# Kernel tuning notes

Hardware: AMD Instinct MI355X
Metric: run time of the kernel (lower is better)

The kernel has to match this reference:

```python
import jax, jax.numpy as jnp
import numpy as np

ALPHA = 0.2          # LeakyReLU negative slope
MASK_VAL = -9e15     # matches torch -9000000000000000.0


def setup_inputs() -> dict:
    key = jax.random.key(0)
    k1, k2, k3, k4 = jax.random.split(key, 4)
    B, N, F_IN, F_OUT, DEG = 64, 1024, 64, 64, 8
    atoms = jax.random.normal(k1, (B, N, F_IN), dtype=jnp.float32)
    edges = jax.random.randint(k2, (B, N, DEG), 0, N, dtype=jnp.int64)
    # xavier_uniform with gain=1.414
    def xavier(k, shape, gain=1.414):
        fan_in, fan_out = shape[0], shape[1]
        bound = gain * np.sqrt(6.0 / (fan_in + fan_out))
        return jax.random.uniform(k, shape, jnp.float32, -bound, bound)
    W = xavier(k3, (F_IN, F_OUT))
    a = xavier(k4, (2 * F_OUT, 1))
    return {"atoms": atoms, "edges": edges, "W": W, "a": a}


def reference(atoms, edges, W, a):
    B, N, _ = atoms.shape
    F_OUT = W.shape[1]
    # h = atom @ W per graph -> [B, N, F_OUT]
    h = jnp.einsum('bnf,fo->bno', atoms, W)
    # Decompose concat-attention: e_ij = leakyrelu(h_i . a1 + h_j . a2)
    a1 = a[:F_OUT, 0]
    a2 = a[F_OUT:, 0]
    s1 = h @ a1  # [B, N]
    s2 = h @ a2  # [B, N]
    e = s1[:, :, None] + s2[:, None, :]  # [B, N, N]
    e = jnp.where(e > 0, e, ALPHA * e)   # LeakyReLU
    # Build adjacency mask from edge lists: adj[b, i, edges[b,i,d]] = True
    b_idx = jnp.arange(B)[:, None, None]
    i_idx = jnp.arange(N)[None, :, None]
    adj = jnp.zeros((B, N, N), dtype=bool).at[b_idx, i_idx, edges].set(True)
    e = jnp.where(adj, e, MASK_VAL)
    attn = jax.nn.softmax(e, axis=-1)    # [B, N, N]
    h_prime = jnp.einsum('bij,bjo->bio', attn, h)
    return jax.nn.elu(h_prime)
```

## Files before the change

kernel.cpp:

```cpp
#include <hip/hip_runtime.h>
#include <math.h>

#define BATCH 64
#define NNODE 1024
#define FDIM 64
#define DEG 8
#define ALPHA 0.2f

typedef __attribute__((ext_vector_type(8))) short bf16x8;
typedef __attribute__((ext_vector_type(4))) float f32x4;

__device__ __forceinline__ short f2bf(float f) {
    union { float f; unsigned u; } v; v.f = f;
    unsigned r = v.u + 0x7fffu + ((v.u >> 16) & 1u);
    return (short)(r >> 16);
}

__global__ void gat_k0(const float* __restrict__ W, const float* __restrict__ a,
                       float* __restrict__ wa) {
    const int k = threadIdx.x;
    float p1 = 0.f, p2 = 0.f;
    #pragma unroll
    for (int j = 0; j < FDIM; ++j) {
        const float w = W[k * FDIM + j];
        p1 = fmaf(w, a[j], p1);
        p2 = fmaf(w, a[FDIM + j], p2);
    }
    wa[k] = p1; wa[FDIM + k] = p2;
}

__global__ __launch_bounds__(256) void gat_k1(
    const float* __restrict__ atoms,
    const float* __restrict__ W,
    const float* __restrict__ wa,
    float* __restrict__ h,
    float* __restrict__ s1,
    float* __restrict__ s2)
{
    const int lane = threadIdx.x & 63;
    const int wv   = threadIdx.x >> 6;
    const int l16  = lane & 15;
    const int qd   = lane >> 4;
    const int rowbase = (blockIdx.x * 4 + wv) * 16;

    bf16x8 Bw[2][4];
    #pragma unroll
    for (int ks = 0; ks < 2; ++ks)
        #pragma unroll
        for (int t = 0; t < 4; ++t)
            #pragma unroll
            for (int j = 0; j < 8; ++j)
                Bw[ks][t][j] = f2bf(W[(ks * 32 + qd * 8 + j) * FDIM + t * 16 + l16]);

    bf16x8 Bs[2];
    #pragma unroll
    for (int ks = 0; ks < 2; ++ks)
        #pragma unroll
        for (int j = 0; j < 8; ++j) {
            const int k = ks * 32 + qd * 8 + j;
            const float v = (l16 == 0) ? wa[k] : ((l16 == 1) ? wa[FDIM + k] : 0.f);
            Bs[ks][j] = f2bf(v);
        }

    const float* __restrict__ ar = atoms + (size_t)(rowbase + l16) * FDIM;
    bf16x8 A[2];
    #pragma unroll
    for (int ks = 0; ks < 2; ++ks) {
        const float4 p0 = *(const float4*)(ar + ks * 32 + qd * 8);
        const float4 p1 = *(const float4*)(ar + ks * 32 + qd * 8 + 4);
        A[ks][0] = f2bf(p0.x); A[ks][1] = f2bf(p0.y);
        A[ks][2] = f2bf(p0.z); A[ks][3] = f2bf(p0.w);
        A[ks][4] = f2bf(p1.x); A[ks][5] = f2bf(p1.y);
        A[ks][6] = f2bf(p1.z); A[ks][7] = f2bf(p1.w);
    }

    f32x4 C[4] = {{0,0,0,0},{0,0,0,0},{0,0,0,0},{0,0,0,0}};
    f32x4 Cs = {0,0,0,0};
    #pragma unroll
    for (int ks = 0; ks < 2; ++ks) {
        #pragma unroll
        for (int t = 0; t < 4; ++t)
            C[t] = __builtin_amdgcn_mfma_f32_16x16x32_bf16(A[ks], Bw[ks][t], C[t], 0, 0, 0);
        Cs = __builtin_amdgcn_mfma_f32_16x16x32_bf16(A[ks], Bs[ks], Cs, 0, 0, 0);
    }

    #pragma unroll
    for (int t = 0; t < 4; ++t)
        #pragma unroll
        for (int r = 0; r < 4; ++r)
            h[(size_t)(rowbase + qd * 4 + r) * FDIM + t * 16 + l16] = C[t][r];

    if (l16 < 2) {
        float* sp = (l16 == 0) ? s1 : s2;
        #pragma unroll
        for (int r = 0; r < 4; ++r)
            sp[rowbase + qd * 4 + r] = Cs[r];
    }
}

__global__ __launch_bounds__(256) void gat_k2(
    const float* __restrict__ h,
    const float* __restrict__ s1g,
    const float* __restrict__ s2g,
    const int*   __restrict__ edges,
    float* __restrict__ out)
{
    __shared__ float s2l[NNODE];
    __shared__ int   el[64 * DEG];
    __shared__ float s1l[64];

    const int bid   = blockIdx.x;
    const int slot  = bid >> 3;
    const int b     = (bid & 7) + 8 * (slot & 7);
    const int chunk = slot >> 3;
    const int rowbase = b * NNODE + chunk * 64;

    const int tid = threadIdx.x;
    ((float4*)s2l)[tid] = ((const float4*)(s2g + b * NNODE))[tid];
    ((int2*)el)[tid]    = ((const int2*)(edges + (size_t)rowbase * DEG))[tid];
    if (tid < 64) s1l[tid] = s1g[rowbase + tid];
    __syncthreads();

    const int lane = tid & 63;
    const int wv   = tid >> 6;
    const float* __restrict__ hb = h + (size_t)b * NNODE * FDIM;

    #pragma unroll 2
    for (int i = 0; i < 16; ++i) {
        const int rl = wv * 16 + i;
        int ej[DEG];
        #pragma unroll
        for (int k = 0; k < DEG; ++k) ej[k] = el[rl * DEG + k];

        const float si = s1l[rl];
        float e[DEG], mx = -INFINITY;
        #pragma unroll
        for (int k = 0; k < DEG; ++k) {
            float v = si + s2l[ej[k]];
            v = (v > 0.f) ? v : ALPHA * v;
            e[k] = v; mx = fmaxf(mx, v);
        }
        float wgt[DEG], wsum = 0.f;
        #pragma unroll
        for (int k = 0; k < DEG; ++k) {
            bool kp = true;
            #pragma unroll
            for (int m = 0; m < DEG; ++m)
                if (m < k && ej[m] == ej[k]) kp = false;
            const float w = kp ? __expf(e[k] - mx) : 0.f;
            wgt[k] = w; wsum += w;
        }
        const float inv = 1.f / wsum;

        float acc = 0.f;
        #pragma unroll
        for (int k = 0; k < DEG; ++k)
            acc = fmaf(wgt[k] * inv, hb[(size_t)ej[k] * FDIM + lane], acc);

        out[(size_t)(rowbase + rl) * FDIM + lane] = (acc > 0.f) ? acc : (__expf(acc) - 1.f);
    }
}

extern "C" void kernel_launch(void* const* d_in, const int* in_sizes, int n_in,
                              void* d_out, int out_size, void* d_ws, size_t ws_size,
                              hipStream_t stream) {
    const float* atoms = (const float*)d_in[0];
    const int*   edges = (const int*)d_in[1];
    const float* W     = (const float*)d_in[2];
    const float* a     = (const float*)d_in[3];
    float* out = (float*)d_out;

    const int rows = BATCH * NNODE;

    float* h  = (float*)d_ws;
    float* s1 = h + (size_t)rows * FDIM;
    float* s2 = s1 + rows;
    float* wa = s2 + rows;

    gat_k0<<<1, 64, 0, stream>>>(W, a, wa);
    gat_k1<<<rows / 64, 256, 0, stream>>>(atoms, W, wa, h, s1, s2);
    gat_k2<<<rows / 64, 256, 0, stream>>>(h, s1, s2, edges, out);
}
```

Before: 102.7 us.

## Fuse projection, score and attention kernels into one LDS-resident per-graph kernel

```diff
diff --git a/kernel.cpp b/kernel.cpp
--- a/kernel.cpp
+++ b/kernel.cpp
@@ -6,6 +6,8 @@
 #define FDIM 64
 #define DEG 8
 #define ALPHA 0.2f
+#define HSTR 66
+#define WSTR 65
 
 typedef __attribute__((ext_vector_type(8))) short bf16x8;
 typedef __attribute__((ext_vector_type(4))) float f32x4;
@@ -15,33 +17,51 @@
     unsigned r = v.u + 0x7fffu + ((v.u >> 16) & 1u);
     return (short)(r >> 16);
 }
-
-__global__ void gat_k0(const float* __restrict__ W, const float* __restrict__ a,
-                       float* __restrict__ wa) {
-    const int k = threadIdx.x;
-    float p1 = 0.f, p2 = 0.f;
-    #pragma unroll
-    for (int j = 0; j < FDIM; ++j) {
-        const float w = W[k * FDIM + j];
-        p1 = fmaf(w, a[j], p1);
-        p2 = fmaf(w, a[FDIM + j], p2);
-    }
-    wa[k] = p1; wa[FDIM + k] = p2;
+__device__ __forceinline__ float bf2f(unsigned short s) {
+    union { unsigned u; float f; } v; v.u = ((unsigned)s) << 16;
+    return v.f;
 }
 
-__global__ __launch_bounds__(256) void gat_k1(
+__global__ __launch_bounds__(1024) void gat_fused(
     const float* __restrict__ atoms,
+    const int*   __restrict__ edges,
     const float* __restrict__ W,
-    const float* __restrict__ wa,
-    float* __restrict__ h,
-    float* __restrict__ s1,
-    float* __restrict__ s2)
+    const float* __restrict__ a,
+    float* __restrict__ out)
 {
-    const int lane = threadIdx.x & 63;
-    const int wv   = threadIdx.x >> 6;
+    extern __shared__ char smem[];
+    unsigned short* hl  = (unsigned short*)smem;
+    float*          Wl  = (float*)(smem + NNODE * HSTR * 2);
+    float*          s1l = Wl + FDIM * WSTR;
+    float*          s2l = s1l + NNODE;
+    float*          waL = s2l + NNODE;
+
+    const int tid = threadIdx.x;
+    const int bid = blockIdx.x;
+    const int xcd = bid & 7, kk = bid >> 3;
+    const int b     = xcd * 8 + (kk & 7);
+    const int chunk = kk >> 3;
+
+    #pragma unroll
+    for (int i = 0; i < 4; ++i) {
+        const int idx = tid + 1024 * i;
+        Wl[(idx >> 6) * WSTR + (idx & 63)] = W[idx];
+    }
+    __syncthreads();
+
+    const int lane = tid & 63;
+    const int wvu  = __builtin_amdgcn_readfirstlane(tid >> 6);
     const int l16  = lane & 15;
     const int qd   = lane >> 4;
-    const int rowbase = (blockIdx.x * 4 + wv) * 16;
+
+    if (tid < 2 * FDIM) {
+        const int which = tid >> 6, kr = tid & 63;
+        float p = 0.f;
+        #pragma unroll
+        for (int j = 0; j < FDIM; ++j)
+            p = fmaf(Wl[kr * WSTR + j], a[which * FDIM + j], p);
+        waL[which * FDIM + kr] = p;
+    }
 
     bf16x8 Bw[2][4];
     #pragma unroll
@@ -50,7 +70,9 @@
         for (int t = 0; t < 4; ++t)
             #pragma unroll
             for (int j = 0; j < 8; ++j)
-                Bw[ks][t][j] = f2bf(W[(ks * 32 + qd * 8 + j) * FDIM + t * 16 + l16]);
+                Bw[ks][t][j] = f2bf(Wl[(ks * 32 + qd * 8 + j) * WSTR + t * 16 + l16]);
+
+    __syncthreads();
 
     bf16x8 Bs[2];
     #pragma unroll
@@ -58,81 +80,66 @@
         #pragma unroll
         for (int j = 0; j < 8; ++j) {
             const int k = ks * 32 + qd * 8 + j;
-            const float v = (l16 == 0) ? wa[k] : ((l16 == 1) ? wa[FDIM + k] : 0.f);
+            const float v = (l16 == 0) ? waL[k] : ((l16 == 1) ? waL[FDIM + k] : 0.f);
             Bs[ks][j] = f2bf(v);
         }
 
-    const float* __restrict__ ar = atoms + (size_t)(rowbase + l16) * FDIM;
-    bf16x8 A[2];
+    const float* __restrict__ ab = atoms + (size_t)b * NNODE * FDIM;
     #pragma unroll
-    for (int ks = 0; ks < 2; ++ks) {
-        const float4 p0 = *(const float4*)(ar + ks * 32 + qd * 8);
-        const float4 p1 = *(const float4*)(ar + ks * 32 + qd * 8 + 4);
-        A[ks][0] = f2bf(p0.x); A[ks][1] = f2bf(p0.y);
-        A[ks][2] = f2bf(p0.z); A[ks][3] = f2bf(p0.w);
-        A[ks][4] = f2bf(p1.x); A[ks][5] = f2bf(p1.y);
-        A[ks][6] = f2bf(p1.z); A[ks][7] = f2bf(p1.w);
-    }
+    for (int t4 = 0; t4 < 4; ++t4) {
+        const int rowbase = wvu * 64 + t4 * 16;
+        const float* __restrict__ ar = ab + (size_t)(rowbase + l16) * FDIM;
 
-    f32x4 C[4] = {{0,0,0,0},{0,0,0,0},{0,0,0,0},{0,0,0,0}};
-    f32x4 Cs = {0,0,0,0};
-    #pragma unroll
-    for (int ks = 0; ks < 2; ++ks) {
+        bf16x8 A[2];
+        #pragma unroll
+        for (int ks = 0; ks < 2; ++ks) {
+            const float4 p0 = *(const float4*)(ar + ks * 32 + qd * 8);
+            const float4 p1 = *(const float4*)(ar + ks * 32 + qd * 8 + 4);
+            A[ks][0] = f2bf(p0.x); A[ks][1] = f2bf(p0.y);
+            A[ks][2] = f2bf(p0.z); A[ks][3] = f2bf(p0.w);
+            A[ks][4] = f2bf(p1.x); A[ks][5] = f2bf(p1.y);
+            A[ks][6] = f2bf(p1.z); A[ks][7] = f2bf(p1.w);
+        }
+
+        f32x4 C[4] = {{0,0,0,0},{0,0,0,0},{0,0,0,0},{0,0,0,0}};
+        f32x4 Cs = {0,0,0,0};
+        #pragma unroll
+        for (int ks = 0; ks < 2; ++ks) {
+            #pragma unroll
+            for (int t = 0; t < 4; ++t)
+                C[t] = __builtin_amdgcn_mfma_f32_16x16x32_bf16(A[ks], Bw[ks][t], C[t], 0, 0, 0);
+            Cs = __builtin_amdgcn_mfma_f32_16x16x32_bf16(A[ks], Bs[ks], Cs, 0, 0, 0);
+        }
+
         #pragma unroll
         for (int t = 0; t < 4; ++t)
-            C[t] = __builtin_amdgcn_mfma_f32_16x16x32_bf16(A[ks], Bw[ks][t], C[t], 0, 0, 0);
-        Cs = __builtin_amdgcn_mfma_f32_16x16x32_bf16(A[ks], Bs[ks], Cs, 0, 0, 0);
+            #pragma unroll
+            for (int r = 0; r < 4; ++r)
+                hl[(rowbase + qd * 4 + r) * HSTR + t * 16 + l16] =
+                    (unsigned short)f2bf(C[t][r]);
+
+        if (l16 == 0) {
+            #pragma unroll
+            for (int r = 0; r < 4; ++r) s1l[rowbase + qd * 4 + r] = Cs[r];
+        } else if (l16 == 1) {
+            #pragma unroll
+            for (int r = 0; r < 4; ++r) s2l[rowbase + qd * 4 + r] = Cs[r];
+        }
     }
-
-    #pragma unroll
-    for (int t = 0; t < 4; ++t)
-        #pragma unroll
-        for (int r = 0; r < 4; ++r)
-            h[(size_t)(rowbase + qd * 4 + r) * FDIM + t * 16 + l16] = C[t][r];
-
-    if (l16 < 2) {
-        float* sp = (l16 == 0) ? s1 : s2;
-        #pragma unroll
-        for (int r = 0; r < 4; ++r)
-            sp[rowbase + qd * 4 + r] = Cs[r];
-    }
-}
-
-__global__ __launch_bounds__(256) void gat_k2(
-    const float* __restrict__ h,
-    const float* __restrict__ s1g,
-    const float* __restrict__ s2g,
-    const int*   __restrict__ edges,
-    float* __restrict__ out)
-{
-    __shared__ float s2l[NNODE];
-    __shared__ int   el[64 * DEG];
-    __shared__ float s1l[64];
-
-    const int bid   = blockIdx.x;
-    const int slot  = bid >> 3;
-    const int b     = (bid & 7) + 8 * (slot & 7);
-    const int chunk = slot >> 3;
-    const int rowbase = b * NNODE + chunk * 64;
-
-    const int tid = threadIdx.x;
-    ((float4*)s2l)[tid] = ((const float4*)(s2g + b * NNODE))[tid];
-    ((int2*)el)[tid]    = ((const int2*)(edges + (size_t)rowbase * DEG))[tid];
-    if (tid < 64) s1l[tid] = s1g[rowbase + tid];
     __syncthreads();
 
-    const int lane = tid & 63;
-    const int wv   = tid >> 6;
-    const float* __restrict__ hb = h + (size_t)b * NNODE * FDIM;
-
+    const int nodebase = chunk * 256 + wvu * 16;
     #pragma unroll 2
     for (int i = 0; i < 16; ++i) {
-        const int rl = wv * 16 + i;
+        const int node = nodebase + i;
+        const int grow = b * NNODE + node;
+
         int ej[DEG];
+        const int* __restrict__ ep = edges + (size_t)grow * DEG;
         #pragma unroll
-        for (int k = 0; k < DEG; ++k) ej[k] = el[rl * DEG + k];
+        for (int k = 0; k < DEG; ++k) ej[k] = ep[k];
 
-        const float si = s1l[rl];
+        const float si = s1l[node];
         float e[DEG], mx = -INFINITY;
         #pragma unroll
         for (int k = 0; k < DEG; ++k) {
@@ -155,9 +162,9 @@
         float acc = 0.f;
         #pragma unroll
         for (int k = 0; k < DEG; ++k)
-            acc = fmaf(wgt[k] * inv, hb[(size_t)ej[k] * FDIM + lane], acc);
+            acc = fmaf(wgt[k] * inv, bf2f(hl[ej[k] * HSTR + lane]), acc);
 
-        out[(size_t)(rowbase + rl) * FDIM + lane] = (acc > 0.f) ? acc : (__expf(acc) - 1.f);
+        out[(size_t)grow * FDIM + lane] = (acc > 0.f) ? acc : (__expf(acc) - 1.f);
     }
 }
 
@@ -170,14 +177,9 @@
     const float* a     = (const float*)d_in[3];
     float* out = (float*)d_out;
 
-    const int rows = BATCH * NNODE;
+    const size_t lds_bytes =
+        (size_t)NNODE * HSTR * 2 +
+        ((size_t)FDIM * WSTR + 2 * NNODE + 2 * FDIM) * 4;
 
-    float* h  = (float*)d_ws;
-    float* s1 = h + (size_t)rows * FDIM;
-    float* s2 = s1 + rows;
-    float* wa = s2 + rows;
-
-    gat_k0<<<1, 64, 0, stream>>>(W, a, wa);
-    gat_k1<<<rows / 64, 256, 0, stream>>>(atoms, W, wa, h, s1, s2);
-    gat_k2<<<rows / 64, 256, 0, stream>>>(h, s1, s2, edges, out);
+    gat_fused<<<BATCH * 4, 1024, lds_bytes, stream>>>(atoms, edges, W, a, out);
 }
```

New measurement: 103.7 us. Within noise of the previous version (+1.0%).
